# Kernel optimization log

Hardware: AMD Instinct MI355X
Metric: run time of the kernel (lower is better)

## Reference

```python
import jax, jax.numpy as jnp
import numpy as np

B, L, D, F, E, K = 2, 2048, 1024, 4096, 8, 2


def setup_inputs() -> dict:
    key = jax.random.key(0)
    ks = jax.random.split(key, 8)
    s = 0.02
    return {
        "x": jax.random.normal(ks[0], (B, L, D), dtype=jnp.float32),
        "Wg": jax.random.normal(ks[1], (D, E), dtype=jnp.float32) * s,
        "bg": jnp.zeros((E,), dtype=jnp.float32),
        "W1": jax.random.normal(ks[2], (E, D, F), dtype=jnp.float32) * s,
        "b1": jnp.zeros((E, F), dtype=jnp.float32),
        "W2": jax.random.normal(ks[3], (E, F, D), dtype=jnp.float32) * s,
        "b2": jnp.zeros((E, D), dtype=jnp.float32),
    }


def reference(x, Wg, bg, W1, b1, W2, b2):
    num_experts = Wg.shape[1]
    gate_scores = x @ Wg + bg                                # [B,L,E]
    topk_scores, topk_ids = jax.lax.top_k(gate_scores, K)    # [B,L,K]
    topk_weights = jax.nn.softmax(topk_scores, axis=-1)      # [B,L,K]
    gate_probs = jax.nn.softmax(gate_scores, axis=-1)        # [B,L,E]

    onehot = jax.nn.one_hot(topk_ids, num_experts, dtype=x.dtype)  # [B,L,K,E]
    expert_mask = onehot.sum(axis=2)                         # [B,L,E]
    freq = expert_mask.mean(axis=(0, 1))                     # [E]
    prob_mean = gate_probs.mean(axis=(0, 1))                 # [E]
    load_balance_loss = num_experts * jnp.sum(freq * prob_mean)

    # combine weight per token per expert (0 if expert not selected)
    combine = jnp.sum(onehot * topk_weights[..., None], axis=2)    # [B,L,E]

    # dense dispatch: run every expert FFN on all tokens, weight & combine
    h = jnp.einsum('bld,edf->belf', x, W1) + b1[None, :, None, :]  # [B,E,L,F]
    h = jax.nn.gelu(h, approximate=False)                          # exact GELU (torch default)
    y = jnp.einsum('belf,efd->beld', h, W2) + b2[None, :, None, :] # [B,E,L,D]
    out = jnp.einsum('ble,beld->bld', combine, y)                  # [B,L,D]
    return out, load_balance_loss
```

## Files before the change

kernel.cpp:

```cpp
#include <hip/hip_runtime.h>
#include <hip/hip_bf16.h>
#include <cstdint>
#include <cstddef>

#define B_ 2
#define L_ 2048
#define D_ 1024
#define F_ 4096
#define E_ 8
#define NTOK 4096
#define MAXROWS 9216
#define MAXMT 72

typedef __hip_bfloat16 bf16;
typedef __attribute__((ext_vector_type(8))) short short8;
typedef __attribute__((ext_vector_type(4))) float floatx4;

typedef const __attribute__((address_space(1))) uint32_t* gptr_t;
typedef __attribute__((address_space(3))) uint32_t* lptr_t;

__device__ __forceinline__ void async_load16(const bf16* gp, bf16* lp) {
    __builtin_amdgcn_global_load_lds((gptr_t)(const void*)gp, (lptr_t)(void*)lp, 16, 0, 0);
}

__device__ __forceinline__ uint16_t bfbits(bf16 h) {
    union { bf16 b; uint16_t u; } v; v.b = h; return v.u;
}
__device__ __forceinline__ uint32_t pack2(float a, float b) {
    return (uint32_t)bfbits(__float2bfloat16(a)) | ((uint32_t)bfbits(__float2bfloat16(b)) << 16);
}
__device__ __forceinline__ float ublo(uint32_t u){ return __uint_as_float(u << 16); }
__device__ __forceinline__ float ubhi(uint32_t u){ return __uint_as_float(u & 0xffff0000u); }

__device__ __forceinline__ float fast_gelu(float x) {
    float x2 = x * x;
    float z = x * fmaf(0.1029432f, x2, 2.3022081f);
    z = fminf(z, 120.f);
    float u = __builtin_amdgcn_exp2f(z);
    return x * u * __builtin_amdgcn_rcpf(1.f + u);
}

__global__ __launch_bounds__(256) void gate_kernel(
    const float* __restrict__ x, const float* __restrict__ Wg,
    const float* __restrict__ bg, float* __restrict__ psum_pad,
    uint32_t* __restrict__ top_ids, float* __restrict__ top_w)
{
    __shared__ float psum_l[E_];
    int t = threadIdx.x;
    if (t < E_) psum_l[t] = 0.f;
    __syncthreads();

    int wave = t >> 6, lane = t & 63;
    for (int j = 0; j < 4; ++j) {
        int token = blockIdx.x * 16 + wave * 4 + j;
        const float* xr = x + (size_t)token * D_;

        float acc[E_];
#pragma unroll
        for (int e = 0; e < E_; ++e) acc[e] = 0.f;
#pragma unroll
        for (int i = 0; i < 4; ++i) {
            int d = lane * 4 + 256 * i;
            float4 xv = *(const float4*)(xr + d);
            const float* xs = &xv.x;
#pragma unroll
            for (int jj = 0; jj < 4; ++jj) {
                const float4* wr4 = (const float4*)(Wg + (size_t)(d + jj) * E_);
                float4 wa = wr4[0], wb = wr4[1];
                float xvj = xs[jj];
                acc[0] += xvj * wa.x;  acc[1] += xvj * wa.y;
                acc[2] += xvj * wa.z;  acc[3] += xvj * wa.w;
                acc[4] += xvj * wb.x;  acc[5] += xvj * wb.y;
                acc[6] += xvj * wb.z;  acc[7] += xvj * wb.w;
            }
        }
#pragma unroll
        for (int off = 32; off >= 1; off >>= 1) {
#pragma unroll
            for (int e = 0; e < E_; ++e) acc[e] += __shfl_xor(acc[e], off, 64);
        }
        if (lane == 0) {
            float s[E_];
#pragma unroll
            for (int e = 0; e < E_; ++e) s[e] = acc[e] + bg[e];
            int i0 = 0;
#pragma unroll
            for (int e = 1; e < E_; ++e) if (s[e] > s[i0]) i0 = e;
            int i1 = -1;
#pragma unroll
            for (int e = 0; e < E_; ++e) {
                if (e == i0) continue;
                if (i1 < 0 || s[e] > s[i1]) i1 = e;
            }
            float e1 = expf(s[i1] - s[i0]);
            float w0 = 1.f / (1.f + e1);
            float w1 = e1 * w0;
            top_ids[token] = (uint32_t)i0 | ((uint32_t)i1 << 8);
            top_w[token]        = w0;
            top_w[NTOK + token] = w1;

            float mx = s[i0], p[E_], sum = 0.f;
#pragma unroll
            for (int e = 0; e < E_; ++e) { p[e] = expf(s[e] - mx); sum += p[e]; }
            float inv = 1.f / sum;
#pragma unroll
            for (int e = 0; e < E_; ++e) atomicAdd(&psum_l[e], p[e] * inv);
        }
    }
    __syncthreads();
    if (t < E_) atomicAdd(&psum_pad[t * 32], psum_l[t]);
}

__global__ __launch_bounds__(256) void compact_kernel(
    const uint32_t* __restrict__ top_ids, const float* __restrict__ top_w,
    int* __restrict__ cnt, int* __restrict__ tok_list, float* __restrict__ w_list,
    int* __restrict__ rowid)
{
    int e = blockIdx.x;
    int t = threadIdx.x, wave = t >> 6, lane = t & 63;
    __shared__ int wcnt[4];
    int base = 0;
    for (int r0 = 0; r0 < NTOK; r0 += 256) {
        int token = r0 + t;
        uint32_t ids = top_ids[token];
        int slot = -1;
        if ((int)(ids & 255u) == e) slot = 0;
        else if ((int)((ids >> 8) & 255u) == e) slot = 1;
        unsigned long long mask = __ballot(slot >= 0);
        int lpos = __popcll(mask & ((1ull << lane) - 1ull));
        if (lane == 0) wcnt[wave] = (int)__popcll(mask);
        __syncthreads();
        int woff = 0, tot = 0;
#pragma unroll
        for (int w2 = 0; w2 < 4; ++w2) { if (w2 < wave) woff += wcnt[w2]; tot += wcnt[w2]; }
        if (slot >= 0) {
            int pos = base + woff + lpos;
            tok_list[e*NTOK + pos] = token;
            w_list[e*NTOK + pos]   = top_w[slot*NTOK + token];
            rowid[slot*NTOK + token] = (e << 13) | pos;
        }
        base += tot;
        __syncthreads();
    }
    if (t == 0) cnt[e] = base;
}

__global__ void finalize_gate_kernel(const int* __restrict__ cnt, const float* __restrict__ psum_pad,
                                     int* __restrict__ off, float* __restrict__ loss_out,
                                     int* __restrict__ mt_map, int* __restrict__ mt_hdr)
{
    int o = 0; float Ls = 0.f; int g = 0;
    for (int e = 0; e < E_; ++e) {
        off[e] = o;
        int mt = (cnt[e] + 127) >> 7;
        for (int m = 0; m < mt; ++m) mt_map[g++] = (e << 8) | m;
        o += mt << 7;
        Ls += (float)cnt[e] * psum_pad[e * 32];
    }
    mt_hdr[0] = g;
    mt_hdr[1] = (g + 7) >> 3;
    loss_out[0] = (float)E_ * Ls / ((float)NTOK * (float)NTOK);
}

__global__ __launch_bounds__(256) void transpose_bf16_kernel(
    const float* __restrict__ in, bf16* __restrict__ outp, int R, int C)
{
    int tilesR = R >> 6, tilesC = C >> 6;
    int per = tilesR * tilesC;
    int bx = blockIdx.x;
    int e  = bx / per; int r2 = bx % per;
    int tr = r2 / tilesC, tc = r2 % tilesC;
    int r0 = tr << 6, c0 = tc << 6;
    const float* ip = in  + (size_t)e * R * C;
    bf16*        op = outp + (size_t)e * R * C;

    __shared__ uint32_t T[64][36];
    int t = threadIdx.x;
    int rp = t >> 4;
    int c4 = (t & 15) * 4;

#pragma unroll
    for (int it = 0; it < 2; ++it) {
        int pr = rp + 16 * it;
        const float* p = ip + (size_t)(r0 + 2*pr) * C + c0 + c4;
        float4 a = *(const float4*)(p);
        float4 b = *(const float4*)(p + C);
        T[c4+0][pr] = pack2(a.x, b.x);
        T[c4+1][pr] = pack2(a.y, b.y);
        T[c4+2][pr] = pack2(a.z, b.z);
        T[c4+3][pr] = pack2(a.w, b.w);
    }
    __syncthreads();

    int s     = t & 7;
    int cbase = t >> 3;
#pragma unroll
    for (int pass = 0; pass < 2; ++pass) {
        int cc = cbase + 32 * pass;
        uint4 u = *(const uint4*)&T[cc][4*s];
        *(uint4*)(op + (size_t)(c0 + cc) * R + r0 + 8*s) = u;
    }
}

__global__ __launch_bounds__(256) void gather_kernel(
    const float* __restrict__ x, const int* __restrict__ cnt, const int* __restrict__ off,
    const int* __restrict__ tok_list, bf16* __restrict__ Xg)
{
    int bx = blockIdx.x;
    int e  = bx >> 12;
    int i  = bx & 4095;
    if (i >= cnt[e]) return;
    int tok = tok_list[e*NTOK + i];
    size_t row = (size_t)(off[e] + i);
    int t = threadIdx.x;
    float4 v = *(const float4*)(x + (size_t)tok * D_ + t*4);
    uint2 uu;
    uu.x = pack2(v.x, v.y);
    uu.y = pack2(v.z, v.w);
    *(uint2*)(Xg + row * D_ + t*4) = uu;
}

__global__ __launch_bounds__(256) void gemm1_kernel(
    const bf16* __restrict__ Xg, const bf16* __restrict__ W1t,
    const float* __restrict__ b1, const int* __restrict__ cnt,
    const int* __restrict__ off, bf16* __restrict__ H)
{
    int bx = blockIdx.x;
    int e  = bx >> 10;
    int r2 = bx & 1023;
    int mtile = r2 >> 5, ntile = r2 & 31;
    int n = cnt[e];
    if (mtile * 128 >= n) return;
    int row0 = off[e] + mtile * 128;
    int f0 = ntile * 128;

    __shared__ bf16 As[128*64];
    __shared__ bf16 Bs[128*64];

    int t = threadIdx.x;
    int wave = t >> 6, lane = t & 63;
    int wm = wave & 1, wn = wave >> 1;
    int q = lane >> 4, ln = lane & 15;
    int sm = lane >> 3, sc = lane & 7;

    const bf16* Abase = Xg  + (size_t)row0 * D_;
    const bf16* Bbase = W1t + ((size_t)e * F_ + f0) * D_;

    floatx4 acc[4][4];
#pragma unroll
    for (int mt = 0; mt < 4; ++mt)
#pragma unroll
        for (int nt = 0; nt < 4; ++nt) acc[mt][nt] = {0.f, 0.f, 0.f, 0.f};

    for (int kt = 0; kt < D_; kt += 64) {
        __syncthreads();
#pragma unroll
        for (int i = 0; i < 4; ++i) {
            int g = wave*4 + i;
            int m = g*8 + sm;
            int ca = sc ^ (m & 7);
            async_load16(Abase + (size_t)m * D_ + kt + ca*8, &As[g*512]);
            async_load16(Bbase + (size_t)m * D_ + kt + ca*8, &Bs[g*512]);
        }
        __syncthreads();
#pragma unroll
        for (int kk = 0; kk < 2; ++kk) {
            short8 av[4], bv[4];
#pragma unroll
            for (int mt = 0; mt < 4; ++mt) {
                int r = wm*64 + mt*16 + ln;
                int cs = (kk*4 + q) ^ (r & 7);
                av[mt] = *(const short8*)&As[r*64 + cs*8];
            }
#pragma unroll
            for (int nt = 0; nt < 4; ++nt) {
                int r = wn*64 + nt*16 + ln;
                int cs = (kk*4 + q) ^ (r & 7);
                bv[nt] = *(const short8*)&Bs[r*64 + cs*8];
            }
#pragma unroll
            for (int mt = 0; mt < 4; ++mt)
#pragma unroll
                for (int nt = 0; nt < 4; ++nt)
                    acc[mt][nt] = __builtin_amdgcn_mfma_f32_16x16x32_bf16(av[mt], bv[nt], acc[mt][nt], 0, 0, 0);
        }
    }

#pragma unroll
    for (int nt = 0; nt < 4; ++nt) {
        int f = f0 + wn*64 + nt*16 + ln;
        float b1v = b1[(size_t)e * F_ + f];
#pragma unroll
        for (int mt = 0; mt < 4; ++mt) {
            int rl = wm*64 + mt*16 + q*4;
#pragma unroll
            for (int r = 0; r < 4; ++r) {
                float v = acc[mt][nt][r] + b1v;
                H[(size_t)(row0 + rl + r) * F_ + f] = __float2bfloat16(fast_gelu(v));
            }
        }
    }
}

__global__ __launch_bounds__(256) void gemm2_kernel(
    const bf16* __restrict__ H, const bf16* __restrict__ W2t,
    const float* __restrict__ b2, const int* __restrict__ cnt, const int* __restrict__ off,
    const int* __restrict__ mt_map, const int* __restrict__ mt_hdr,
    bf16* __restrict__ Y)
{
    int bx = blockIdx.x;
    int k  = bx & 7;
    int j  = bx >> 3;
    int jj = j >> 4;
    int ntile = j & 15;
    int nmt = mt_hdr[0], qc = mt_hdr[1];
    if (jj >= qc) return;
    int mt = k * qc + jj;
    if (mt >= nmt) return;
    int em = mt_map[mt];
    int e = em >> 8, mtile = em & 255;
    int n = cnt[e];
    int row0 = off[e] + mtile * 128;
    int d0 = ntile * 64;

    __shared__ bf16 As[128*64];
    __shared__ bf16 Bs[64*64];

    int t = threadIdx.x;
    int wave = t >> 6, lane = t & 63;
    int wm = wave & 1, wn = wave >> 1;
    int q = lane >> 4, ln = lane & 15;
    int sm = lane >> 3, sc = lane & 7;

    const bf16* Abase = H   + (size_t)row0 * F_;
    const bf16* Bbase = W2t + ((size_t)e * D_ + d0) * F_;

    floatx4 acc[4][2];
#pragma unroll
    for (int mt2 = 0; mt2 < 4; ++mt2)
#pragma unroll
        for (int nt = 0; nt < 2; ++nt) acc[mt2][nt] = {0.f, 0.f, 0.f, 0.f};

    for (int kt = 0; kt < F_; kt += 64) {
        __syncthreads();
#pragma unroll
        for (int i = 0; i < 4; ++i) {
            int g = wave*4 + i;
            int m = g*8 + sm;
            int ca = sc ^ (m & 7);
            async_load16(Abase + (size_t)m * F_ + kt + ca*8, &As[g*512]);
        }
#pragma unroll
        for (int i = 0; i < 2; ++i) {
            int g = wave*2 + i;
            int m = g*8 + sm;
            int ca = sc ^ (m & 7);
            async_load16(Bbase + (size_t)m * F_ + kt + ca*8, &Bs[g*512]);
        }
        __syncthreads();
#pragma unroll
        for (int kk = 0; kk < 2; ++kk) {
            short8 av[4], bv[2];
#pragma unroll
            for (int mt2 = 0; mt2 < 4; ++mt2) {
                int r = wm*64 + mt2*16 + ln;
                int cs = (kk*4 + q) ^ (r & 7);
                av[mt2] = *(const short8*)&As[r*64 + cs*8];
            }
#pragma unroll
            for (int nt = 0; nt < 2; ++nt) {
                int r = wn*32 + nt*16 + ln;
                int cs = (kk*4 + q) ^ (r & 7);
                bv[nt] = *(const short8*)&Bs[r*64 + cs*8];
            }
#pragma unroll
            for (int mt2 = 0; mt2 < 4; ++mt2)
#pragma unroll
                for (int nt = 0; nt < 2; ++nt)
                    acc[mt2][nt] = __builtin_amdgcn_mfma_f32_16x16x32_bf16(av[mt2], bv[nt], acc[mt2][nt], 0, 0, 0);
        }
    }

    float b2v[2];
#pragma unroll
    for (int nt = 0; nt < 2; ++nt)
        b2v[nt] = b2[(size_t)e * D_ + d0 + wn*32 + nt*16 + ln];

#pragma unroll
    for (int mt2 = 0; mt2 < 4; ++mt2) {
#pragma unroll
        for (int r = 0; r < 4; ++r) {
            int loc = wm*64 + mt2*16 + q*4 + r;
            int i = mtile*128 + loc;
            if (i < n) {
                bf16* yp = Y + (size_t)(row0 + loc) * D_ + d0;
#pragma unroll
                for (int nt = 0; nt < 2; ++nt)
                    yp[wn*32 + nt*16 + ln] = __float2bfloat16(acc[mt2][nt][r] + b2v[nt]);
            }
        }
    }
}

__global__ __launch_bounds__(256) void combine_kernel(
    const bf16* __restrict__ Y, const int* __restrict__ rowid,
    const float* __restrict__ top_w, const int* __restrict__ off,
    float* __restrict__ out)
{
    int tok = blockIdx.x;
    int t = threadIdx.x;
    int v0 = rowid[tok], v1 = rowid[NTOK + tok];
    float w0 = top_w[tok], w1 = top_w[NTOK + tok];
    size_t r0 = (size_t)(off[v0 >> 13] + (v0 & 8191));
    size_t r1 = (size_t)(off[v1 >> 13] + (v1 & 8191));
    uint2 a = *(const uint2*)(Y + r0 * D_ + t*4);
    uint2 b = *(const uint2*)(Y + r1 * D_ + t*4);
    float4 o;
    o.x = w0 * ublo(a.x) + w1 * ublo(b.x);
    o.y = w0 * ubhi(a.x) + w1 * ubhi(b.x);
    o.z = w0 * ublo(a.y) + w1 * ublo(b.y);
    o.w = w0 * ubhi(a.y) + w1 * ubhi(b.y);
    *(float4*)(out + (size_t)tok * D_ + t*4) = o;
}

extern "C" void kernel_launch(void* const* d_in, const int* in_sizes, int n_in,
                              void* d_out, int out_size, void* d_ws, size_t ws_size,
                              hipStream_t stream)
{
    const float* x  = (const float*)d_in[0];
    const float* Wg = (const float*)d_in[1];
    const float* bg = (const float*)d_in[2];
    const float* W1 = (const float*)d_in[3];
    const float* b1 = (const float*)d_in[4];
    const float* W2 = (const float*)d_in[5];
    const float* b2 = (const float*)d_in[6];
    float* out = (float*)d_out;

    char* ws = (char*)d_ws;
    int*      cnt      = (int*)(ws + 0);
    int*      off      = (int*)(ws + 128);
    int*      mt_map   = (int*)(ws + 256);
    int*      mt_hdr   = (int*)(ws + 576);
    float*    psum_pad = (float*)(ws + 1024);
    uint32_t* top_ids  = (uint32_t*)(ws + 8192);
    float*    top_w    = (float*)(ws + 8192 + 16384);
    int*      tok_list = (int*)(ws + 65536);
    float*    w_list   = (float*)(ws + 65536 + 131072);
    int*      rowid    = (int*)(ws + 327680);
    size_t o = 1u << 20;
    bf16*  W1t = (bf16*)(ws + o);  o += (size_t)E_ * D_ * F_ * 2;
    bf16*  W2t = (bf16*)(ws + o);  o += (size_t)E_ * F_ * D_ * 2;
    bf16*  Xg  = (bf16*)(ws + o);  o += (size_t)MAXROWS * D_ * 2;
    bf16*  H   = (bf16*)(ws + o);
    bf16*  Y   = Xg;

    hipMemsetAsync(ws + 1024, 0, 1024, stream);

    transpose_bf16_kernel<<<E_ * 16 * 64, 256, 0, stream>>>(W1, W1t, D_, F_);
    transpose_bf16_kernel<<<E_ * 64 * 16, 256, 0, stream>>>(W2, W2t, F_, D_);

    gate_kernel<<<256, 256, 0, stream>>>(x, Wg, bg, psum_pad, top_ids, top_w);
    compact_kernel<<<E_, 256, 0, stream>>>(top_ids, top_w, cnt, tok_list, w_list, rowid);
    finalize_gate_kernel<<<1, 1, 0, stream>>>(cnt, psum_pad, off, out + (size_t)NTOK * D_, mt_map, mt_hdr);
    gather_kernel<<<E_ * 4096, 256, 0, stream>>>(x, cnt, off, tok_list, Xg);

    gemm1_kernel<<<E_ * 32 * 32, 256, 0, stream>>>(Xg, W1t, b1, cnt, off, H);
    gemm2_kernel<<<MAXMT * 16, 256, 0, stream>>>(H, W2t, b2, cnt, off, mt_map, mt_hdr, Y);
    combine_kernel<<<NTOK, 256, 0, stream>>>(Y, rowid, top_w, off, out);
}
```

Before: 627.5 us.

## Fuse compact/finalize/gather into one dispatch kernel and scatter-add combine into GEMM2

Replaces the serial per-expert compact kernel, the single-thread finalize kernel and the gather kernel with one 256-block dispatch kernel. Each block redundantly computes the expert histogram and offsets, then gathers the rows whose index maps to it. The GEMM2 epilogue now weights its results and atomically adds them into a zeroed fp32 output, which removes the Y buffer and the combine kernel. The two weight transposes are merged into one launch. The costs are a full output memset, float atomics with nondeterministic summation order, and repeated scan work in every dispatch block.

```diff
diff --git a/kernel.cpp b/kernel.cpp
--- a/kernel.cpp
+++ b/kernel.cpp
@@ -29,8 +29,6 @@
 __device__ __forceinline__ uint32_t pack2(float a, float b) {
     return (uint32_t)bfbits(__float2bfloat16(a)) | ((uint32_t)bfbits(__float2bfloat16(b)) << 16);
 }
-__device__ __forceinline__ float ublo(uint32_t u){ return __uint_as_float(u << 16); }
-__device__ __forceinline__ float ubhi(uint32_t u){ return __uint_as_float(u & 0xffff0000u); }
 
 __device__ __forceinline__ float fast_gelu(float x) {
     float x2 = x * x;
@@ -111,64 +109,132 @@
     if (t < E_) atomicAdd(&psum_pad[t * 32], psum_l[t]);
 }
 
-__global__ __launch_bounds__(256) void compact_kernel(
-    const uint32_t* __restrict__ top_ids, const float* __restrict__ top_w,
-    int* __restrict__ cnt, int* __restrict__ tok_list, float* __restrict__ w_list,
-    int* __restrict__ rowid)
-{
-    int e = blockIdx.x;
+__global__ __launch_bounds__(256) void dispatch_kernel(
+    const float* __restrict__ x, const uint32_t* __restrict__ top_ids,
+    const float* __restrict__ top_w, const float* __restrict__ psum_pad,
+    int* __restrict__ cnt, int* __restrict__ off_g,
+    int* __restrict__ mt_map, int* __restrict__ mt_hdr,
+    int* __restrict__ tok_row, float* __restrict__ w_row,
+    bf16* __restrict__ Xg, float* __restrict__ loss_out)
+{
+    __shared__ int cnt_l[E_];
+    __shared__ int off_l[E_];
+    __shared__ int base_l[E_];
+    __shared__ int wcnt[E_][4];
+    __shared__ int qrow[64];
+    __shared__ int qtok[64];
+    __shared__ float qw[64];
+    __shared__ int qn;
+
     int t = threadIdx.x, wave = t >> 6, lane = t & 63;
-    __shared__ int wcnt[4];
-    int base = 0;
-    for (int r0 = 0; r0 < NTOK; r0 += 256) {
-        int token = r0 + t;
+    int bid = blockIdx.x;
+    if (t < E_) cnt_l[t] = 0;
+    if (t == 0) qn = 0;
+    __syncthreads();
+
+    uint32_t myids[16];
+    int lc[E_];
+#pragma unroll
+    for (int e = 0; e < E_; ++e) lc[e] = 0;
+#pragma unroll
+    for (int c = 0; c < 16; ++c) {
+        int token = c * 256 + t;
         uint32_t ids = top_ids[token];
-        int slot = -1;
-        if ((int)(ids & 255u) == e) slot = 0;
-        else if ((int)((ids >> 8) & 255u) == e) slot = 1;
-        unsigned long long mask = __ballot(slot >= 0);
-        int lpos = __popcll(mask & ((1ull << lane) - 1ull));
-        if (lane == 0) wcnt[wave] = (int)__popcll(mask);
-        __syncthreads();
-        int woff = 0, tot = 0;
-#pragma unroll
-        for (int w2 = 0; w2 < 4; ++w2) { if (w2 < wave) woff += wcnt[w2]; tot += wcnt[w2]; }
-        if (slot >= 0) {
-            int pos = base + woff + lpos;
-            tok_list[e*NTOK + pos] = token;
-            w_list[e*NTOK + pos]   = top_w[slot*NTOK + token];
-            rowid[slot*NTOK + token] = (e << 13) | pos;
-        }
-        base += tot;
-        __syncthreads();
-    }
-    if (t == 0) cnt[e] = base;
-}
-
-__global__ void finalize_gate_kernel(const int* __restrict__ cnt, const float* __restrict__ psum_pad,
-                                     int* __restrict__ off, float* __restrict__ loss_out,
-                                     int* __restrict__ mt_map, int* __restrict__ mt_hdr)
-{
-    int o = 0; float Ls = 0.f; int g = 0;
+        myids[c] = ids;
+        int e0 = (int)(ids & 255u), e1 = (int)((ids >> 8) & 255u);
+#pragma unroll
+        for (int e = 0; e < E_; ++e) lc[e] += (e0 == e) + (e1 == e);
+    }
+#pragma unroll
     for (int e = 0; e < E_; ++e) {
-        off[e] = o;
-        int mt = (cnt[e] + 127) >> 7;
-        for (int m = 0; m < mt; ++m) mt_map[g++] = (e << 8) | m;
-        o += mt << 7;
-        Ls += (float)cnt[e] * psum_pad[e * 32];
-    }
-    mt_hdr[0] = g;
-    mt_hdr[1] = (g + 7) >> 3;
-    loss_out[0] = (float)E_ * Ls / ((float)NTOK * (float)NTOK);
-}
-
-__global__ __launch_bounds__(256) void transpose_bf16_kernel(
-    const float* __restrict__ in, bf16* __restrict__ outp, int R, int C)
-{
+        int v = lc[e];
+#pragma unroll
+        for (int off = 32; off >= 1; off >>= 1) v += __shfl_xor(v, off, 64);
+        if (lane == 0) atomicAdd(&cnt_l[e], v);
+    }
+    __syncthreads();
+
+    if (t == 0) {
+        int o = 0;
+#pragma unroll
+        for (int e = 0; e < E_; ++e) { off_l[e] = o; o += (cnt_l[e] + 127) & ~127; }
+    }
+    if (t < E_) base_l[t] = 0;
+    __syncthreads();
+
+    if (bid == 0 && t == 0) {
+        int g = 0;
+        for (int e = 0; e < E_; ++e) {
+            cnt[e] = cnt_l[e]; off_g[e] = off_l[e];
+            int mtn = (cnt_l[e] + 127) >> 7;
+            for (int m = 0; m < mtn; ++m) mt_map[g++] = (e << 8) | m;
+        }
+        mt_hdr[0] = g;
+        mt_hdr[1] = (g + 7) >> 3;
+        float Ls = 0.f;
+        for (int e = 0; e < E_; ++e) Ls += (float)cnt_l[e] * psum_pad[e * 32];
+        loss_out[0] = (float)E_ * Ls / ((float)NTOK * (float)NTOK);
+    }
+
+#pragma unroll
+    for (int c = 0; c < 16; ++c) {
+        uint32_t ids = myids[c];
+        int e0 = (int)(ids & 255u), e1 = (int)((ids >> 8) & 255u);
+        int lp0 = 0, lp1 = 0;
+#pragma unroll
+        for (int e = 0; e < E_; ++e) {
+            bool m = (e0 == e) || (e1 == e);
+            unsigned long long mk = __ballot(m);
+            if (lane == 0) wcnt[e][wave] = (int)__popcll(mk);
+            int lp = (int)__popcll(mk & ((1ull << lane) - 1ull));
+            if (e0 == e) lp0 = lp;
+            if (e1 == e) lp1 = lp;
+        }
+        __syncthreads();
+        int woff0 = 0, woff1 = 0;
+#pragma unroll
+        for (int w2 = 0; w2 < 4; ++w2) {
+            if (w2 < wave) { woff0 += wcnt[e0][w2]; woff1 += wcnt[e1][w2]; }
+        }
+        int token = c * 256 + t;
+        int row0 = off_l[e0] + base_l[e0] + woff0 + lp0;
+        int row1 = off_l[e1] + base_l[e1] + woff1 + lp1;
+        if ((row0 & 255) == bid) {
+            int qi = atomicAdd(&qn, 1);
+            qrow[qi] = row0; qtok[qi] = token; qw[qi] = top_w[token];
+        }
+        if ((row1 & 255) == bid) {
+            int qi = atomicAdd(&qn, 1);
+            qrow[qi] = row1; qtok[qi] = token; qw[qi] = top_w[NTOK + token];
+        }
+        __syncthreads();
+        if (t < E_) base_l[t] += wcnt[t][0] + wcnt[t][1] + wcnt[t][2] + wcnt[t][3];
+        __syncthreads();
+    }
+
+    int nq = qn;
+    for (int i = 0; i < nq; ++i) {
+        int row = qrow[i]; int tok = qtok[i];
+        float4 v = *(const float4*)(x + (size_t)tok * D_ + t * 4);
+        uint2 uu;
+        uu.x = pack2(v.x, v.y);
+        uu.y = pack2(v.z, v.w);
+        *(uint2*)(Xg + (size_t)row * D_ + t * 4) = uu;
+        if (t == 0) { tok_row[row] = tok; w_row[row] = qw[i]; }
+    }
+}
+
+__global__ __launch_bounds__(256) void transpose_both_kernel(
+    const float* __restrict__ W1, const float* __restrict__ W2,
+    bf16* __restrict__ W1t, bf16* __restrict__ W2t)
+{
+    int bx = blockIdx.x;
+    const float* in; bf16* outp; int R, C, idx;
+    if (bx < E_ * 1024) { in = W1; outp = W1t; R = D_; C = F_; idx = bx; }
+    else                { in = W2; outp = W2t; R = F_; C = D_; idx = bx - E_ * 1024; }
     int tilesR = R >> 6, tilesC = C >> 6;
     int per = tilesR * tilesC;
-    int bx = blockIdx.x;
-    int e  = bx / per; int r2 = bx % per;
+    int e  = idx / per; int r2 = idx % per;
     int tr = r2 / tilesC, tc = r2 % tilesC;
     int r0 = tr << 6, c0 = tc << 6;
     const float* ip = in  + (size_t)e * R * C;
@@ -202,24 +268,6 @@
     }
 }
 
-__global__ __launch_bounds__(256) void gather_kernel(
-    const float* __restrict__ x, const int* __restrict__ cnt, const int* __restrict__ off,
-    const int* __restrict__ tok_list, bf16* __restrict__ Xg)
-{
-    int bx = blockIdx.x;
-    int e  = bx >> 12;
-    int i  = bx & 4095;
-    if (i >= cnt[e]) return;
-    int tok = tok_list[e*NTOK + i];
-    size_t row = (size_t)(off[e] + i);
-    int t = threadIdx.x;
-    float4 v = *(const float4*)(x + (size_t)tok * D_ + t*4);
-    uint2 uu;
-    uu.x = pack2(v.x, v.y);
-    uu.y = pack2(v.z, v.w);
-    *(uint2*)(Xg + row * D_ + t*4) = uu;
-}
-
 __global__ __launch_bounds__(256) void gemm1_kernel(
     const bf16* __restrict__ Xg, const bf16* __restrict__ W1t,
     const float* __restrict__ b1, const int* __restrict__ cnt,
@@ -306,7 +354,8 @@
     const bf16* __restrict__ H, const bf16* __restrict__ W2t,
     const float* __restrict__ b2, const int* __restrict__ cnt, const int* __restrict__ off,
     const int* __restrict__ mt_map, const int* __restrict__ mt_hdr,
-    bf16* __restrict__ Y)
+    const int* __restrict__ tok_row, const float* __restrict__ w_row,
+    float* __restrict__ out)
 {
     int bx = blockIdx.x;
     int k  = bx & 7;
@@ -393,34 +442,15 @@
             int loc = wm*64 + mt2*16 + q*4 + r;
             int i = mtile*128 + loc;
             if (i < n) {
-                bf16* yp = Y + (size_t)(row0 + loc) * D_ + d0;
+                int tok = tok_row[row0 + loc];
+                float w = w_row[row0 + loc];
+                float* op = out + (size_t)tok * D_ + d0 + wn*32 + ln;
 #pragma unroll
                 for (int nt = 0; nt < 2; ++nt)
-                    yp[wn*32 + nt*16 + ln] = __float2bfloat16(acc[mt2][nt][r] + b2v[nt]);
-            }
-        }
-    }
-}
-
-__global__ __launch_bounds__(256) void combine_kernel(
-    const bf16* __restrict__ Y, const int* __restrict__ rowid,
-    const float* __restrict__ top_w, const int* __restrict__ off,
-    float* __restrict__ out)
-{
-    int tok = blockIdx.x;
-    int t = threadIdx.x;
-    int v0 = rowid[tok], v1 = rowid[NTOK + tok];
-    float w0 = top_w[tok], w1 = top_w[NTOK + tok];
-    size_t r0 = (size_t)(off[v0 >> 13] + (v0 & 8191));
-    size_t r1 = (size_t)(off[v1 >> 13] + (v1 & 8191));
-    uint2 a = *(const uint2*)(Y + r0 * D_ + t*4);
-    uint2 b = *(const uint2*)(Y + r1 * D_ + t*4);
-    float4 o;
-    o.x = w0 * ublo(a.x) + w1 * ublo(b.x);
-    o.y = w0 * ubhi(a.x) + w1 * ubhi(b.x);
-    o.z = w0 * ublo(a.y) + w1 * ublo(b.y);
-    o.w = w0 * ubhi(a.y) + w1 * ubhi(b.y);
-    *(float4*)(out + (size_t)tok * D_ + t*4) = o;
+                    atomicAdd(op + nt*16, w * (acc[mt2][nt][r] + b2v[nt]));
+            }
+        }
+    }
 }
 
 extern "C" void kernel_launch(void* const* d_in, const int* in_sizes, int n_in,
@@ -444,27 +474,26 @@
     float*    psum_pad = (float*)(ws + 1024);
     uint32_t* top_ids  = (uint32_t*)(ws + 8192);
     float*    top_w    = (float*)(ws + 8192 + 16384);
-    int*      tok_list = (int*)(ws + 65536);
-    float*    w_list   = (float*)(ws + 65536 + 131072);
-    int*      rowid    = (int*)(ws + 327680);
+    int*      tok_row  = (int*)(ws + 65536);
+    float*    w_row    = (float*)(ws + 65536 + 65536);
     size_t o = 1u << 20;
     bf16*  W1t = (bf16*)(ws + o);  o += (size_t)E_ * D_ * F_ * 2;
     bf16*  W2t = (bf16*)(ws + o);  o += (size_t)E_ * F_ * D_ * 2;
     bf16*  Xg  = (bf16*)(ws + o);  o += (size_t)MAXROWS * D_ * 2;
     bf16*  H   = (bf16*)(ws + o);
-    bf16*  Y   = Xg;
 
     hipMemsetAsync(ws + 1024, 0, 1024, stream);
-
-    transpose_bf16_kernel<<<E_ * 16 * 64, 256, 0, stream>>>(W1, W1t, D_, F_);
-    transpose_bf16_kernel<<<E_ * 64 * 16, 256, 0, stream>>>(W2, W2t, F_, D_);
+    hipMemsetAsync(out, 0, (size_t)NTOK * D_ * sizeof(float), stream);
+
+    transpose_both_kernel<<<E_ * 1024 * 2, 256, 0, stream>>>(W1, W2, W1t, W2t);
 
     gate_kernel<<<256, 256, 0, stream>>>(x, Wg, bg, psum_pad, top_ids, top_w);
-    compact_kernel<<<E_, 256, 0, stream>>>(top_ids, top_w, cnt, tok_list, w_list, rowid);
-    finalize_gate_kernel<<<1, 1, 0, stream>>>(cnt, psum_pad, off, out + (size_t)NTOK * D_, mt_map, mt_hdr);
-    gather_kernel<<<E_ * 4096, 256, 0, stream>>>(x, cnt, off, tok_list, Xg);
+    dispatch_kernel<<<256, 256, 0, stream>>>(x, top_ids, top_w, psum_pad,
+                                             cnt, off, mt_map, mt_hdr,
+                                             tok_row, w_row, Xg,
+                                             out + (size_t)NTOK * D_);
 
     gemm1_kernel<<<E_ * 32 * 32, 256, 0, stream>>>(Xg, W1t, b1, cnt, off, H);
-    gemm2_kernel<<<MAXMT * 16, 256, 0, stream>>>(H, W2t, b2, cnt, off, mt_map, mt_hdr, Y);
-    combine_kernel<<<NTOK, 256, 0, stream>>>(Y, rowid, top_w, off, out);
-}
+    gemm2_kernel<<<MAXMT * 16, 256, 0, stream>>>(H, W2t, b2, cnt, off, mt_map, mt_hdr,
+                                                 tok_row, w_row, out);
+}
```

After: 653.3 us. 1.04x slower.
